# Optimization experiments

Hardware: AMD Instinct MI355X
Metric: run time of the kernel (lower is better)

Reference implementation:

```python
import jax, jax.numpy as jnp
import numpy as np

N, E = 50000, 800000
IN, HID, HEADS, OUT = 128, 16, 4, 40
NEG_SLOPE = 0.2
BN_EPS = 1e-5


def gat_conv(x, edge_src, edge_dst, W, a_src, a_dst, b, heads, out_ch, concat):
    """PyG GATConv: linear -> per-head attention logits -> segment softmax over
    incoming edges of each target node -> weighted scatter-sum. Self-loops are
    assumed already appended to edge_src/edge_dst."""
    n = x.shape[0]
    h = (x @ W.T).reshape(n, heads, out_ch)              # [N, H, C]
    alpha_s = jnp.sum(h * a_src, axis=-1)                # [N, H]
    alpha_d = jnp.sum(h * a_dst, axis=-1)                # [N, H]
    logits = jax.nn.leaky_relu(alpha_s[edge_src] + alpha_d[edge_dst], NEG_SLOPE)  # [E', H]
    # numerically-stable segment softmax over edges grouped by target node
    seg_max = jax.ops.segment_max(logits, edge_dst, num_segments=n)
    e = jnp.exp(logits - seg_max[edge_dst])
    seg_sum = jax.ops.segment_sum(e, edge_dst, num_segments=n)
    alpha = e / (seg_sum[edge_dst] + 1e-16)              # [E', H]
    msg = h[edge_src] * alpha[:, :, None]                # [E', H, C]
    out = jax.ops.segment_sum(msg, edge_dst, num_segments=n)  # [N, H, C]
    out = out.reshape(n, heads * out_ch) if concat else out.mean(axis=1)
    return out + b


def batch_norm(x, gamma, beta):
    mean = x.mean(axis=0)
    var = x.var(axis=0)  # biased, matching torch BN normalization
    return (x - mean) * jax.lax.rsqrt(var + BN_EPS) * gamma + beta


def setup_inputs() -> dict:
    key = jax.random.key(0)
    ks = jax.random.split(key, 16)
    H = HID * HEADS  # 64
    inp = {
        "x": jax.random.normal(ks[0], (N, IN), jnp.float32),
        "edge_index": jax.random.randint(ks[1], (2, E), 0, N, jnp.int64),
        # layer 0: IN -> HID, HEADS heads, concat
        "W0": jax.random.normal(ks[2], (H, IN), jnp.float32) * 0.05,
        "a_src0": jax.random.normal(ks[3], (1, HEADS, HID), jnp.float32) * 0.05,
        "a_dst0": jax.random.normal(ks[4], (1, HEADS, HID), jnp.float32) * 0.05,
        "b0": jnp.zeros((H,), jnp.float32),
        # layer 1: H -> HID, HEADS heads, concat
        "W1": jax.random.normal(ks[5], (H, H), jnp.float32) * 0.05,
        "a_src1": jax.random.normal(ks[6], (1, HEADS, HID), jnp.float32) * 0.05,
        "a_dst1": jax.random.normal(ks[7], (1, HEADS, HID), jnp.float32) * 0.05,
        "b1": jnp.zeros((H,), jnp.float32),
        # layer 2: H -> OUT, 1 head, concat=False
        "W2": jax.random.normal(ks[8], (OUT, H), jnp.float32) * 0.05,
        "a_src2": jax.random.normal(ks[9], (1, 1, OUT), jnp.float32) * 0.05,
        "a_dst2": jax.random.normal(ks[10], (1, 1, OUT), jnp.float32) * 0.05,
        "b2": jnp.zeros((OUT,), jnp.float32),
        # batchnorms
        "g0": jnp.ones((H,), jnp.float32), "bt0": jnp.zeros((H,), jnp.float32),
        "g1": jnp.ones((H,), jnp.float32), "bt1": jnp.zeros((H,), jnp.float32),
    }
    return inp


def reference(x, edge_index, W0, a_src0, a_dst0, b0, W1, a_src1, a_dst1, b1,
              W2, a_src2, a_dst2, b2, g0, bt0, g1, bt1):
    n = x.shape[0]
    loop = jnp.arange(n, dtype=edge_index.dtype)
    src = jnp.concatenate([edge_index[0], loop])  # PyG add_self_loops=True
    dst = jnp.concatenate([edge_index[1], loop])

    h = gat_conv(x, src, dst, W0, a_src0, a_dst0, b0, HEADS, HID, True)
    h = batch_norm(h, g0, bt0)
    h = gat_conv(h, src, dst, W1, a_src1, a_dst1, b1, HEADS, HID, True)
    h = batch_norm(h, g1, bt1)
    emb = gat_conv(h, src, dst, W2, a_src2, a_dst2, b2, 1, OUT, False)
    return jax.nn.log_softmax(emb, axis=1), emb
```

## Files before the change

### kernel.cpp

```cpp
#include <hip/hip_runtime.h>
#include <hip/hip_bf16.h>
#include <math.h>

#define NN 50000
#define NE 800000
#define CURPAD 16
#define CAP 64

using short8 = __attribute__((ext_vector_type(8))) short;
using f32x4  = __attribute__((ext_vector_type(4))) float;

__device__ inline short bfbits(float f) {
    __hip_bfloat16 b = __float2bfloat16(f);
    return __builtin_bit_cast(short, b);
}
__device__ inline short8 cvt8(float4 lo, float4 hi) {
    short8 r;
    r[0] = bfbits(lo.x); r[1] = bfbits(lo.y); r[2] = bfbits(lo.z); r[3] = bfbits(lo.w);
    r[4] = bfbits(hi.x); r[5] = bfbits(hi.y); r[6] = bfbits(hi.z); r[7] = bfbits(hi.w);
    return r;
}

template<int K, int CT, int COUT, int HEADSN, bool FUSESCAT, bool BF16IN>
__global__ __launch_bounds__(256) void mfma_gemm(
    const void* __restrict__ xv, const void* __restrict__ Wv,
    const float* __restrict__ cb,
    const float* __restrict__ a_src, const float* __restrict__ a_dst,
    ushort* __restrict__ h, float* __restrict__ as_out, float* __restrict__ ad_out,
    int n, int scat_blocks,
    const int* __restrict__ esrc, const int* __restrict__ edst,
    int* __restrict__ cnt, unsigned* __restrict__ pk2)
{
    if (FUSESCAT && (int)blockIdx.x < scat_blocks) {
        int base = ((int)blockIdx.x * 256 + (int)threadIdx.x) * 8;
        int d[8], sv[8], pv[8];
#pragma unroll
        for (int j = 0; j < 8; j++) {
            d[j] = (base + j < NE) ? edst[base + j] : -1;
            sv[j] = (base + j < NE) ? esrc[base + j] : 0;
        }
#pragma unroll
        for (int j = 0; j < 8; j++)
            pv[j] = (d[j] >= 0) ? atomicAdd(&cnt[(size_t)d[j] * CURPAD], 1) : 0;
#pragma unroll
        for (int j = 0; j < 8; j++)
            if (d[j] >= 0 && pv[j] < CAP)
                pk2[((size_t)d[j] << 6) + pv[j]] = (unsigned)sv[j];
        return;
    }

    int bid = (int)blockIdx.x - (FUSESCAT ? scat_blocks : 0);
    int tid = threadIdx.x;
    int w = tid >> 6, l = tid & 63;
    int l15 = l & 15, g = l >> 4;
    int m_base = bid * 64 + w * 16;

    f32x4 acc[CT];
#pragma unroll
    for (int ct = 0; ct < CT; ct++) acc[ct] = f32x4{0.f, 0.f, 0.f, 0.f};

    int arow = m_base + l15; if (arow >= n) arow = n - 1;

#pragma unroll
    for (int ks = 0; ks < K / 32; ks++) {
        int k0 = ks * 32 + g * 8;
        short8 a;
        if (BF16IN) {
            const ushort* xrow = (const ushort*)xv + (size_t)arow * K;
            a = *(const short8*)(xrow + k0);
        } else {
            const float* xrow = (const float*)xv + (size_t)arow * K;
            float4 lo = *(const float4*)(xrow + k0);
            float4 hi = *(const float4*)(xrow + k0 + 4);
            a = cvt8(lo, hi);
        }
#pragma unroll
        for (int ct = 0; ct < CT; ct++) {
            int wrow = ct * 16 + l15;
            if (wrow >= COUT) wrow = COUT - 1;
            short8 b;
            if (BF16IN) {
                const ushort* Wr = (const ushort*)Wv + (size_t)wrow * K;
                b = *(const short8*)(Wr + k0);
            } else {
                const float* Wr = (const float*)Wv + (size_t)wrow * K;
                float4 blo = *(const float4*)(Wr + k0);
                float4 bhi = *(const float4*)(Wr + k0 + 4);
                b = cvt8(blo, bhi);
            }
            acc[ct] = __builtin_amdgcn_mfma_f32_16x16x32_bf16(a, b, acc[ct], 0, 0, 0);
        }
    }

    float cbv[CT];
#pragma unroll
    for (int ct = 0; ct < CT; ct++) {
        int col = ct * 16 + l15;
        cbv[ct] = (BF16IN && cb) ? cb[(col < COUT) ? col : (COUT - 1)] : 0.f;
    }

#pragma unroll
    for (int ct = 0; ct < CT; ct++) {
#pragma unroll
        for (int r = 0; r < 4; r++) {
            int row = m_base + g * 4 + r;
            int col = ct * 16 + l15;
            if (row < n && col < COUT)
                h[(size_t)row * COUT + col] = (ushort)bfbits(acc[ct][r] + cbv[ct]);
        }
    }

    if (HEADSN == 4) {
        float asv[CT], adv[CT];
#pragma unroll
        for (int ct = 0; ct < CT; ct++) {
            asv[ct] = a_src[ct * 16 + l15];
            adv[ct] = a_dst[ct * 16 + l15];
        }
#pragma unroll
        for (int r = 0; r < 4; r++) {
            float rs[CT], rd[CT];
#pragma unroll
            for (int ct = 0; ct < CT; ct++) {
                float hv = acc[ct][r] + cbv[ct];
                rs[ct] = hv * asv[ct];
                rd[ct] = hv * adv[ct];
            }
#pragma unroll
            for (int off = 1; off < 16; off <<= 1) {
#pragma unroll
                for (int ct = 0; ct < CT; ct++) {
                    rs[ct] += __shfl_xor(rs[ct], off);
                    rd[ct] += __shfl_xor(rd[ct], off);
                }
            }
            int row = m_base + g * 4 + r;
            if (row < n) {
#pragma unroll
                for (int ct = 0; ct < CT; ct++) {
                    if (l15 == ct) {
                        as_out[row * 4 + ct] = rs[ct];
                        ad_out[row * 4 + ct] = rd[ct];
                    }
                }
            }
        }
    } else {
        float asv[CT], adv[CT];
#pragma unroll
        for (int ct = 0; ct < CT; ct++) {
            int col = ct * 16 + l15;
            asv[ct] = (col < COUT) ? a_src[col] : 0.f;
            adv[ct] = (col < COUT) ? a_dst[col] : 0.f;
        }
#pragma unroll
        for (int r = 0; r < 4; r++) {
            float rs = 0.f, rd = 0.f;
#pragma unroll
            for (int ct = 0; ct < CT; ct++) {
                float hv = acc[ct][r] + cbv[ct];
                rs += hv * asv[ct];
                rd += hv * adv[ct];
            }
#pragma unroll
            for (int off = 1; off < 16; off <<= 1) {
                rs += __shfl_xor(rs, off);
                rd += __shfl_xor(rd, off);
            }
            int row = m_base + g * 4 + r;
            if (row < n && l15 == 0) {
                as_out[row] = rs;
                ad_out[row] = rd;
            }
        }
    }
}

template<int CH, int HEADSN, bool LSM, bool BNP>
__global__ __launch_bounds__(256) void gat_kernel(
    const ushort* __restrict__ h, const float* __restrict__ as,
    const float* __restrict__ ad, const int* __restrict__ cnt,
    const unsigned* __restrict__ pk2, const float* __restrict__ bias,
    float* __restrict__ outf, ushort* __restrict__ outb,
    float* __restrict__ psum, float* __restrict__ psq, int n)
{
    __shared__ float lsv[4][64];
    int tid = threadIdx.x;
    int w = tid >> 6;
    int wid = blockIdx.x * 4 + w;
    int lane = tid & 63;
    int sub = lane & 7, eslot = lane >> 3;
    int c0 = sub * 8;
    bool act = (c0 < CH);
    int hd = (HEADSN == 1) ? 0 : (sub >> 1);
    float adi = ad[wid * HEADSN + hd];

    float ac0 = 0.f, ac1 = 0.f, ac2 = 0.f, ac3 = 0.f;
    float ac4 = 0.f, ac5 = 0.f, ac6 = 0.f, ac7 = 0.f;
    float ss = 0.f;

    int deg = cnt[(size_t)wid * CURPAD];
    if (deg > CAP) deg = CAP;
    int slotbase = wid << 6;
    int nit = (deg + 7) >> 3;
    int pos = eslot;

    bool ok0 = pos < deg;
    int s0 = 0; float av0 = 0.f;
    if (ok0) { s0 = (int)pk2[slotbase + pos]; av0 = as[s0 * HEADSN + hd]; }
    bool ok1 = (pos + 8) < deg;
    int s1 = 0; float av1 = 0.f;
    if (ok1) { s1 = (int)pk2[slotbase + pos + 8]; av1 = as[s1 * HEADSN + hd]; }
    uint4 h0 = make_uint4(0, 0, 0, 0);
    if (ok0 && act) h0 = *(const uint4*)&h[(size_t)s0 * CH + c0];

    for (int it = 0; it < nit; ++it) {
        int pos2 = pos + 16;
        bool ok2 = pos2 < deg;
        int s2 = 0; float av2 = 0.f;
        if (ok2) { s2 = (int)pk2[slotbase + pos2]; av2 = as[s2 * HEADSN + hd]; }
        uint4 h1 = make_uint4(0, 0, 0, 0);
        if (ok1 && act) h1 = *(const uint4*)&h[(size_t)s1 * CH + c0];

        float p = 0.f;
        if (ok0) {
            float lg = av0 + adi;
            lg = (lg > 0.f) ? lg : 0.2f * lg;
            p = __expf(fminf(lg, 60.f));
        }
        ss += p;
        ac0 += p * __uint_as_float(h0.x << 16);
        ac1 += p * __uint_as_float(h0.x & 0xffff0000u);
        ac2 += p * __uint_as_float(h0.y << 16);
        ac3 += p * __uint_as_float(h0.y & 0xffff0000u);
        ac4 += p * __uint_as_float(h0.z << 16);
        ac5 += p * __uint_as_float(h0.z & 0xffff0000u);
        ac6 += p * __uint_as_float(h0.w << 16);
        ac7 += p * __uint_as_float(h0.w & 0xffff0000u);

        s0 = s1; av0 = av1; ok0 = ok1;
        s1 = s2; av1 = av2; ok1 = ok2;
        h0 = h1; pos += 8;
    }

#pragma unroll
    for (int o = 8; o <= 32; o <<= 1) {
        ss  += __shfl_xor(ss, o);
        ac0 += __shfl_xor(ac0, o);  ac1 += __shfl_xor(ac1, o);
        ac2 += __shfl_xor(ac2, o);  ac3 += __shfl_xor(ac3, o);
        ac4 += __shfl_xor(ac4, o);  ac5 += __shfl_xor(ac5, o);
        ac6 += __shfl_xor(ac6, o);  ac7 += __shfl_xor(ac7, o);
    }

    {
        float lg = as[wid * HEADSN + hd] + adi;
        lg = (lg > 0.f) ? lg : 0.2f * lg;
        float ps = __expf(fminf(lg, 60.f));
        ss += ps;
        if (act) {
            uint4 u = *(const uint4*)&h[(size_t)wid * CH + c0];
            ac0 += ps * __uint_as_float(u.x << 16);
            ac1 += ps * __uint_as_float(u.x & 0xffff0000u);
            ac2 += ps * __uint_as_float(u.y << 16);
            ac3 += ps * __uint_as_float(u.y & 0xffff0000u);
            ac4 += ps * __uint_as_float(u.z << 16);
            ac5 += ps * __uint_as_float(u.z & 0xffff0000u);
            ac6 += ps * __uint_as_float(u.w << 16);
            ac7 += ps * __uint_as_float(u.w & 0xffff0000u);
        }
    }

    float inv = 1.f / (ss + 1e-16f);
    float4 bv0 = make_float4(0.f, 0.f, 0.f, 0.f), bv1 = bv0;
    if (act) {
        bv0 = *(const float4*)&bias[c0];
        bv1 = *(const float4*)&bias[c0 + 4];
    }
    float v0 = ac0 * inv + bv0.x;
    float v1 = ac1 * inv + bv0.y;
    float v2 = ac2 * inv + bv0.z;
    float v3 = ac3 * inv + bv0.w;
    float v4 = ac4 * inv + bv1.x;
    float v5 = ac5 * inv + bv1.y;
    float v6 = ac6 * inv + bv1.z;
    float v7 = ac7 * inv + bv1.w;

    if (BNP) {
        if (eslot == 0) {
            lsv[w][c0 + 0] = v0; lsv[w][c0 + 1] = v1;
            lsv[w][c0 + 2] = v2; lsv[w][c0 + 3] = v3;
            lsv[w][c0 + 4] = v4; lsv[w][c0 + 5] = v5;
            lsv[w][c0 + 6] = v6; lsv[w][c0 + 7] = v7;
        }
        __syncthreads();
        if (tid < 64) {
            float a0 = lsv[0][tid], a1 = lsv[1][tid], a2 = lsv[2][tid], a3 = lsv[3][tid];
            psum[(size_t)blockIdx.x * 64 + tid] = (a0 + a1) + (a2 + a3);
            psq[(size_t)blockIdx.x * 64 + tid]  = (a0 * a0 + a1 * a1) + (a2 * a2 + a3 * a3);
        }
    }

    if (LSM) {
        float mx = act ? fmaxf(fmaxf(fmaxf(v0, v1), fmaxf(v2, v3)),
                               fmaxf(fmaxf(v4, v5), fmaxf(v6, v7))) : -INFINITY;
        for (int o = 4; o >= 1; o >>= 1) mx = fmaxf(mx, __shfl_xor(mx, o));
        float sse = 0.f;
        if (act)
            sse = __expf(v0 - mx) + __expf(v1 - mx) + __expf(v2 - mx) + __expf(v3 - mx)
                + __expf(v4 - mx) + __expf(v5 - mx) + __expf(v6 - mx) + __expf(v7 - mx);
        for (int o = 4; o >= 1; o >>= 1) sse += __shfl_xor(sse, o);
        float ls = logf(sse);
        if (eslot == 0 && act) {
            *(float4*)&outf[(size_t)wid * CH + c0] =
                make_float4(v0 - mx - ls, v1 - mx - ls, v2 - mx - ls, v3 - mx - ls);
            *(float4*)&outf[(size_t)wid * CH + c0 + 4] =
                make_float4(v4 - mx - ls, v5 - mx - ls, v6 - mx - ls, v7 - mx - ls);
            *(float4*)&outf[(size_t)n * CH + (size_t)wid * CH + c0] =
                make_float4(v0, v1, v2, v3);
            *(float4*)&outf[(size_t)n * CH + (size_t)wid * CH + c0 + 4] =
                make_float4(v4, v5, v6, v7);
        }
    } else {
        if (eslot == 0 && act) {
            short8 r;
            r[0] = bfbits(v0); r[1] = bfbits(v1); r[2] = bfbits(v2); r[3] = bfbits(v3);
            r[4] = bfbits(v4); r[5] = bfbits(v5); r[6] = bfbits(v6); r[7] = bfbits(v7);
            *(short8*)&outb[(size_t)wid * CH + c0] = r;
        }
    }
}

__global__ __launch_bounds__(256) void bn_reduce(
    const float* __restrict__ psum, const float* __restrict__ psq,
    const float* __restrict__ g, const float* __restrict__ bt,
    float* __restrict__ sc, float* __restrict__ sh, int nb, int n)
{
    int c = blockIdx.x;
    int t = threadIdx.x;
    float s = 0.f, s2 = 0.f;
    for (int r = t; r < nb; r += 256) {
        s  += psum[(size_t)r * 64 + c];
        s2 += psq[(size_t)r * 64 + c];
    }
    __shared__ float a[256], b[256];
    a[t] = s; b[t] = s2; __syncthreads();
    for (int o = 128; o >= 1; o >>= 1) {
        if (t < o) { a[t] += a[t + o]; b[t] += b[t + o]; }
        __syncthreads();
    }
    if (t == 0) {
        float mean = a[0] / n;
        float var = b[0] / n - mean * mean;
        float invs = rsqrtf(var + 1e-5f);
        float scale = g[c] * invs;
        sc[c] = scale;
        sh[c] = bt[c] - mean * scale;
    }
}

__global__ __launch_bounds__(256) void bn_fold(
    const float* __restrict__ sc, const float* __restrict__ sh,
    const float* __restrict__ W, ushort* __restrict__ Wb,
    float* __restrict__ cb, int cout, int k)
{
    int t = threadIdx.x;
    for (int idx = t; idx < cout * k; idx += 256) {
        int kk = idx % k;
        Wb[idx] = (ushort)bfbits(W[idx] * sc[kk]);
    }
    if (t < cout) {
        float s = 0.f;
        for (int kk = 0; kk < k; kk++) s += sh[kk] * W[t * k + kk];
        cb[t] = s;
    }
}

extern "C" void kernel_launch(void* const* d_in, const int* in_sizes, int n_in,
                              void* d_out, int out_size, void* d_ws, size_t ws_size,
                              hipStream_t stream) {
    const float* x   = (const float*)d_in[0];
    const int*   ei  = (const int*)d_in[1];
    const float* W0  = (const float*)d_in[2];
    const float* as0 = (const float*)d_in[3];
    const float* ad0 = (const float*)d_in[4];
    const float* b0  = (const float*)d_in[5];
    const float* W1  = (const float*)d_in[6];
    const float* as1 = (const float*)d_in[7];
    const float* ad1 = (const float*)d_in[8];
    const float* b1  = (const float*)d_in[9];
    const float* W2  = (const float*)d_in[10];
    const float* as2 = (const float*)d_in[11];
    const float* ad2 = (const float*)d_in[12];
    const float* b2  = (const float*)d_in[13];
    const float* g0  = (const float*)d_in[14];
    const float* bt0 = (const float*)d_in[15];
    const float* g1  = (const float*)d_in[16];
    const float* bt1 = (const float*)d_in[17];

    const int* esrc = ei;
    const int* edst = ei + NE;

    char* ws = (char*)d_ws;
    size_t off = 0;
    auto alloc = [&](size_t bytes) {
        void* p = ws + off;
        off += (bytes + 255) & ~(size_t)255;
        return p;
    };
    int* cnt      = (int*)alloc((size_t)NN * CURPAD * 4);
    unsigned* pk2 = (unsigned*)alloc((size_t)NN * CAP * 4);
    ushort* hbuf  = (ushort*)alloc((size_t)NN * 64 * 2);
    ushort* obuf  = (ushort*)alloc((size_t)NN * 64 * 2);
    float* asb    = (float*)alloc((size_t)NN * 4 * 4);
    float* adb    = (float*)alloc((size_t)NN * 4 * 4);
    float* psum   = (float*)alloc((size_t)(NN / 4) * 64 * 4);
    float* psq    = (float*)alloc((size_t)(NN / 4) * 64 * 4);
    float* sc     = (float*)alloc(64 * 4);
    float* sh     = (float*)alloc(64 * 4);
    ushort* W1b   = (ushort*)alloc(64 * 64 * 2);
    ushort* W2b   = (ushort*)alloc(40 * 64 * 2);
    float* cb1    = (float*)alloc(64 * 4);
    float* cb2    = (float*)alloc(40 * 4);

    const int SCB = (NE + 2047) / 2048;
    const int GBM = (NN + 63) / 64;
    const int GB4 = NN / 4;

    hipMemsetAsync(cnt, 0, (size_t)NN * CURPAD * 4, stream);
    mfma_gemm<128, 4, 64, 4, true, false><<<SCB + GBM, 256, 0, stream>>>(
        x, W0, nullptr, as0, ad0, hbuf, asb, adb, NN, SCB,
        esrc, edst, cnt, pk2);

    gat_kernel<64, 4, false, true><<<GB4, 256, 0, stream>>>(
        hbuf, asb, adb, cnt, pk2, b0, nullptr, obuf, psum, psq, NN);
    bn_reduce<<<64, 256, 0, stream>>>(psum, psq, g0, bt0, sc, sh, GB4, NN);
    bn_fold<<<1, 256, 0, stream>>>(sc, sh, W1, W1b, cb1, 64, 64);

    mfma_gemm<64, 4, 64, 4, false, true><<<GBM, 256, 0, stream>>>(
        obuf, W1b, cb1, as1, ad1, hbuf, asb, adb, NN, 0,
        nullptr, nullptr, nullptr, nullptr);
    gat_kernel<64, 4, false, true><<<GB4, 256, 0, stream>>>(
        hbuf, asb, adb, cnt, pk2, b1, nullptr, obuf, psum, psq, NN);
    bn_reduce<<<64, 256, 0, stream>>>(psum, psq, g1, bt1, sc, sh, GB4, NN);
    bn_fold<<<1, 256, 0, stream>>>(sc, sh, W2, W2b, cb2, 40, 64);

    mfma_gemm<64, 3, 40, 1, false, true><<<GBM, 256, 0, stream>>>(
        obuf, W2b, cb2, as2, ad2, hbuf, asb, adb, NN, 0,
        nullptr, nullptr, nullptr, nullptr);
    gat_kernel<40, 1, true, false><<<GB4, 256, 0, stream>>>(
        hbuf, asb, adb, cnt, pk2, b2, (float*)d_out, nullptr, nullptr, nullptr, NN);
}
```

Measured before the change: 252.9 us.

## Replace per-node atomic scatter with two-pass bucketed counting sort into CSR

Swaps the per-edge global atomic scatter into fixed 64-slot per-node arrays for a two-pass bucket sort. Pass one bins edges into 256-node buckets using shared-memory histograms and one global atomic per bucket per block. Pass two, fused into the first GEMM launch, sorts each bucket locally into compact CSR with per-node pointers and degrees. This removes 800k contended global atomics and the padded 64-slot layout, and gives the gather kernels contiguous neighbor lists. The cost is an extra kernel launch plus a fixed per-bucket capacity (BCAP) that silently drops edges if a bucket overflows; in-degree at or below 64 was already assumed before.

```diff
diff --git a/kernel.cpp b/kernel.cpp
--- a/kernel.cpp
+++ b/kernel.cpp
@@ -4,8 +4,9 @@
 
 #define NN 50000
 #define NE 800000
-#define CURPAD 16
-#define CAP 64
+#define NBUCK 196
+#define BCAP 5120
+#define GPAD 16
 
 using short8 = __attribute__((ext_vector_type(8))) short;
 using f32x4  = __attribute__((ext_vector_type(4))) float;
@@ -21,35 +22,82 @@
     return r;
 }
 
-template<int K, int CT, int COUT, int HEADSN, bool FUSESCAT, bool BF16IN>
+__global__ __launch_bounds__(1024) void part1(
+    const int* __restrict__ esrc, const int* __restrict__ edst,
+    int* __restrict__ gcnt, unsigned* __restrict__ bbuf)
+{
+    __shared__ int hist[NBUCK], base[NBUCK], lcur[NBUCK];
+    int t = threadIdx.x;
+    for (int i = t; i < NBUCK; i += 1024) { hist[i] = 0; lcur[i] = 0; }
+    __syncthreads();
+    int base_e = blockIdx.x * 16384;
+    int b_[16]; unsigned pk_[16];
+#pragma unroll
+    for (int j = 0; j < 16; j++) {
+        int e = base_e + j * 1024 + t;
+        if (e < NE) {
+            int d = edst[e];
+            int s = esrc[e];
+            b_[j] = d >> 8;
+            pk_[j] = ((unsigned)s << 8) | (unsigned)(d & 255);
+            atomicAdd(&hist[b_[j]], 1);
+        } else b_[j] = -1;
+    }
+    __syncthreads();
+    for (int i = t; i < NBUCK; i += 1024)
+        base[i] = atomicAdd(&gcnt[i * GPAD], hist[i]);
+    __syncthreads();
+#pragma unroll
+    for (int j = 0; j < 16; j++) {
+        if (b_[j] >= 0) {
+            int pos = base[b_[j]] + atomicAdd(&lcur[b_[j]], 1);
+            if (pos < BCAP) bbuf[(size_t)b_[j] * BCAP + pos] = pk_[j];
+        }
+    }
+}
+
+template<int K, int CT, int COUT, int HEADSN, bool FUSESORT, bool BF16IN>
 __global__ __launch_bounds__(256) void mfma_gemm(
     const void* __restrict__ xv, const void* __restrict__ Wv,
     const float* __restrict__ cb,
     const float* __restrict__ a_src, const float* __restrict__ a_dst,
     ushort* __restrict__ h, float* __restrict__ as_out, float* __restrict__ ad_out,
-    int n, int scat_blocks,
-    const int* __restrict__ esrc, const int* __restrict__ edst,
-    int* __restrict__ cnt, unsigned* __restrict__ pk2)
+    int n,
+    const int* __restrict__ gcnt, const unsigned* __restrict__ bbuf,
+    int* __restrict__ ptr, int* __restrict__ degd, unsigned* __restrict__ csr)
 {
-    if (FUSESCAT && (int)blockIdx.x < scat_blocks) {
-        int base = ((int)blockIdx.x * 256 + (int)threadIdx.x) * 8;
-        int d[8], sv[8], pv[8];
-#pragma unroll
-        for (int j = 0; j < 8; j++) {
-            d[j] = (base + j < NE) ? edst[base + j] : -1;
-            sv[j] = (base + j < NE) ? esrc[base + j] : 0;
-        }
-#pragma unroll
-        for (int j = 0; j < 8; j++)
-            pv[j] = (d[j] >= 0) ? atomicAdd(&cnt[(size_t)d[j] * CURPAD], 1) : 0;
-#pragma unroll
-        for (int j = 0; j < 8; j++)
-            if (d[j] >= 0 && pv[j] < CAP)
-                pk2[((size_t)d[j] << 6) + pv[j]] = (unsigned)sv[j];
+    if (FUSESORT && (int)blockIdx.x < NBUCK) {
+        __shared__ int hist2[256], lcur2[256];
+        int b = blockIdx.x;
+        int t = threadIdx.x;
+        int n_b = gcnt[b * GPAD]; if (n_b > BCAP) n_b = BCAP;
+        hist2[t] = 0;
+        __syncthreads();
+        for (int i = t; i < n_b; i += 256)
+            atomicAdd(&hist2[bbuf[(size_t)b * BCAP + i] & 255u], 1);
+        __syncthreads();
+        int mydeg = hist2[t];
+        for (int off = 1; off < 256; off <<= 1) {
+            int v = (t >= off) ? hist2[t - off] : 0;
+            __syncthreads();
+            hist2[t] += v;
+            __syncthreads();
+        }
+        int excl = hist2[t] - mydeg;
+        lcur2[t] = excl;
+        int node = (b << 8) + t;
+        if (node < NN) { ptr[node] = b * BCAP + excl; degd[node] = mydeg; }
+        __syncthreads();
+        for (int i = t; i < n_b; i += 256) {
+            unsigned pk = bbuf[(size_t)b * BCAP + i];
+            int ln = pk & 255u;
+            int pos = atomicAdd(&lcur2[ln], 1);
+            csr[(size_t)b * BCAP + pos] = pk >> 8;
+        }
         return;
     }
 
-    int bid = (int)blockIdx.x - (FUSESCAT ? scat_blocks : 0);
+    int bid = (int)blockIdx.x - (FUSESORT ? NBUCK : 0);
     int tid = threadIdx.x;
     int w = tid >> 6, l = tid & 63;
     int l15 = l & 15, g = l >> 4;
@@ -179,8 +227,9 @@
 template<int CH, int HEADSN, bool LSM, bool BNP>
 __global__ __launch_bounds__(256) void gat_kernel(
     const ushort* __restrict__ h, const float* __restrict__ as,
-    const float* __restrict__ ad, const int* __restrict__ cnt,
-    const unsigned* __restrict__ pk2, const float* __restrict__ bias,
+    const float* __restrict__ ad, const int* __restrict__ ptr,
+    const int* __restrict__ degd, const unsigned* __restrict__ csr,
+    const float* __restrict__ bias,
     float* __restrict__ outf, ushort* __restrict__ outb,
     float* __restrict__ psum, float* __restrict__ psq, int n)
 {
@@ -199,18 +248,17 @@
     float ac4 = 0.f, ac5 = 0.f, ac6 = 0.f, ac7 = 0.f;
     float ss = 0.f;
 
-    int deg = cnt[(size_t)wid * CURPAD];
-    if (deg > CAP) deg = CAP;
-    int slotbase = wid << 6;
+    int deg = degd[wid];
+    int base = ptr[wid];
     int nit = (deg + 7) >> 3;
     int pos = eslot;
 
     bool ok0 = pos < deg;
     int s0 = 0; float av0 = 0.f;
-    if (ok0) { s0 = (int)pk2[slotbase + pos]; av0 = as[s0 * HEADSN + hd]; }
+    if (ok0) { s0 = (int)csr[base + pos]; av0 = as[s0 * HEADSN + hd]; }
     bool ok1 = (pos + 8) < deg;
     int s1 = 0; float av1 = 0.f;
-    if (ok1) { s1 = (int)pk2[slotbase + pos + 8]; av1 = as[s1 * HEADSN + hd]; }
+    if (ok1) { s1 = (int)csr[base + pos + 8]; av1 = as[s1 * HEADSN + hd]; }
     uint4 h0 = make_uint4(0, 0, 0, 0);
     if (ok0 && act) h0 = *(const uint4*)&h[(size_t)s0 * CH + c0];
 
@@ -218,7 +266,7 @@
         int pos2 = pos + 16;
         bool ok2 = pos2 < deg;
         int s2 = 0; float av2 = 0.f;
-        if (ok2) { s2 = (int)pk2[slotbase + pos2]; av2 = as[s2 * HEADSN + hd]; }
+        if (ok2) { s2 = (int)csr[base + pos2]; av2 = as[s2 * HEADSN + hd]; }
         uint4 h1 = make_uint4(0, 0, 0, 0);
         if (ok1 && act) h1 = *(const uint4*)&h[(size_t)s1 * CH + c0];
 
@@ -407,46 +455,51 @@
         off += (bytes + 255) & ~(size_t)255;
         return p;
     };
-    int* cnt      = (int*)alloc((size_t)NN * CURPAD * 4);
-    unsigned* pk2 = (unsigned*)alloc((size_t)NN * CAP * 4);
-    ushort* hbuf  = (ushort*)alloc((size_t)NN * 64 * 2);
-    ushort* obuf  = (ushort*)alloc((size_t)NN * 64 * 2);
-    float* asb    = (float*)alloc((size_t)NN * 4 * 4);
-    float* adb    = (float*)alloc((size_t)NN * 4 * 4);
-    float* psum   = (float*)alloc((size_t)(NN / 4) * 64 * 4);
-    float* psq    = (float*)alloc((size_t)(NN / 4) * 64 * 4);
-    float* sc     = (float*)alloc(64 * 4);
-    float* sh     = (float*)alloc(64 * 4);
-    ushort* W1b   = (ushort*)alloc(64 * 64 * 2);
-    ushort* W2b   = (ushort*)alloc(40 * 64 * 2);
-    float* cb1    = (float*)alloc(64 * 4);
-    float* cb2    = (float*)alloc(40 * 4);
-
-    const int SCB = (NE + 2047) / 2048;
+    int* gcnt      = (int*)alloc((size_t)NBUCK * GPAD * 4);
+    unsigned* bbuf = (unsigned*)alloc((size_t)NBUCK * BCAP * 4);
+    unsigned* csr  = (unsigned*)alloc((size_t)NBUCK * BCAP * 4);
+    int* ptr       = (int*)alloc((size_t)NN * 4);
+    int* degd      = (int*)alloc((size_t)NN * 4);
+    ushort* hbuf   = (ushort*)alloc((size_t)NN * 64 * 2);
+    ushort* obuf   = (ushort*)alloc((size_t)NN * 64 * 2);
+    float* asb     = (float*)alloc((size_t)NN * 4 * 4);
+    float* adb     = (float*)alloc((size_t)NN * 4 * 4);
+    float* psum    = (float*)alloc((size_t)(NN / 4) * 64 * 4);
+    float* psq     = (float*)alloc((size_t)(NN / 4) * 64 * 4);
+    float* sc      = (float*)alloc(64 * 4);
+    float* sh      = (float*)alloc(64 * 4);
+    ushort* W1b    = (ushort*)alloc(64 * 64 * 2);
+    ushort* W2b    = (ushort*)alloc(40 * 64 * 2);
+    float* cb1     = (float*)alloc(64 * 4);
+    float* cb2     = (float*)alloc(40 * 4);
+
+    const int P1B = (NE + 16383) / 16384;
     const int GBM = (NN + 63) / 64;
     const int GB4 = NN / 4;
 
-    hipMemsetAsync(cnt, 0, (size_t)NN * CURPAD * 4, stream);
-    mfma_gemm<128, 4, 64, 4, true, false><<<SCB + GBM, 256, 0, stream>>>(
-        x, W0, nullptr, as0, ad0, hbuf, asb, adb, NN, SCB,
-        esrc, edst, cnt, pk2);
+    hipMemsetAsync(gcnt, 0, (size_t)NBUCK * GPAD * 4, stream);
+    part1<<<P1B, 1024, 0, stream>>>(esrc, edst, gcnt, bbuf);
+    mfma_gemm<128, 4, 64, 4, true, false><<<NBUCK + GBM, 256, 0, stream>>>(
+        x, W0, nullptr, as0, ad0, hbuf, asb, adb, NN,
+        gcnt, bbuf, ptr, degd, csr);
 
     gat_kernel<64, 4, false, true><<<GB4, 256, 0, stream>>>(
-        hbuf, asb, adb, cnt, pk2, b0, nullptr, obuf, psum, psq, NN);
+        hbuf, asb, adb, ptr, degd, csr, b0, nullptr, obuf, psum, psq, NN);
     bn_reduce<<<64, 256, 0, stream>>>(psum, psq, g0, bt0, sc, sh, GB4, NN);
     bn_fold<<<1, 256, 0, stream>>>(sc, sh, W1, W1b, cb1, 64, 64);
 
     mfma_gemm<64, 4, 64, 4, false, true><<<GBM, 256, 0, stream>>>(
-        obuf, W1b, cb1, as1, ad1, hbuf, asb, adb, NN, 0,
-        nullptr, nullptr, nullptr, nullptr);
+        obuf, W1b, cb1, as1, ad1, hbuf, asb, adb, NN,
+        nullptr, nullptr, nullptr, nullptr, nullptr);
     gat_kernel<64, 4, false, true><<<GB4, 256, 0, stream>>>(
-        hbuf, asb, adb, cnt, pk2, b1, nullptr, obuf, psum, psq, NN);
+        hbuf, asb, adb, ptr, degd, csr, b1, nullptr, obuf, psum, psq, NN);
     bn_reduce<<<64, 256, 0, stream>>>(psum, psq, g1, bt1, sc, sh, GB4, NN);
     bn_fold<<<1, 256, 0, stream>>>(sc, sh, W2, W2b, cb2, 40, 64);
 
     mfma_gemm<64, 3, 40, 1, false, true><<<GBM, 256, 0, stream>>>(
-        obuf, W2b, cb2, as2, ad2, hbuf, asb, adb, NN, 0,
-        nullptr, nullptr, nullptr, nullptr);
+        obuf, W2b, cb2, as2, ad2, hbuf, asb, adb, NN,
+        nullptr, nullptr, nullptr, nullptr, nullptr);
     gat_kernel<40, 1, true, false><<<GB4, 256, 0, stream>>>(
-        hbuf, asb, adb, cnt, pk2, b2, (float*)d_out, nullptr, nullptr, nullptr, NN);
-}
+        hbuf, asb, adb, ptr, degd, csr, b2, (float*)d_out, nullptr,
+        nullptr, nullptr, NN);
+}
```

Result: faster. 241.2 us (-4.6%).
